# Optimization experiments

Hardware: AMD Instinct MI355X
Metric: run time of the kernel (lower is better)

Reference implementation:

```python
import jax, jax.numpy as jnp
import numpy as np

M_ROWS, K, N = 4096, 4096, 4096
DIVFACTOR = 1.0 / (127.0 * 127.0)


def setup_inputs() -> dict:
    key = jax.random.key(0)
    k1, k2, k3, k4, k5 = jax.random.split(key, 5)
    # quantized activations and weights, int8 range
    x = jax.random.randint(k1, (M_ROWS, K), -128, 128, dtype=jnp.int32).astype(jnp.int8)
    scale_x = jnp.abs(jax.random.normal(k2, (M_ROWS,), dtype=jnp.float32)) * 0.01
    weight_int8 = jax.random.randint(k3, (N, K), -128, 128, dtype=jnp.int32).astype(jnp.int8)
    scale_w = jnp.abs(jax.random.normal(k4, (N,), dtype=jnp.float32)) * 0.01
    bias = (jax.random.normal(k5, (N,), dtype=jnp.float32) * 0.01).astype(jnp.float16)
    return {"x": x, "scale_x": scale_x, "weight_int8": weight_int8, "scale_w": scale_w, "bias": bias}


def reference(x, scale_x, weight_int8, scale_w, bias):
    # int8 @ int8^T accumulated (reference path computes in fp32, like torch .float())
    acc = jnp.matmul(x.astype(jnp.float32), weight_int8.T.astype(jnp.float32))  # [M, N]
    out = scale_w[None, :] * (scale_x[:, None] * (acc * DIVFACTOR))
    out = out + bias[None, :].astype(jnp.float32)  # bias promoted fp16->fp32, as in torch
    return out.astype(jnp.float16)
```

## Files before the change

kernel.cpp:

```cpp
#include <hip/hip_runtime.h>
#include <hip/hip_fp16.h>

typedef int v4i __attribute__((ext_vector_type(4)));
typedef const unsigned __attribute__((address_space(1)))* gas_t;
typedef unsigned __attribute__((address_space(3)))* las_t;

#define DIVFACTOR (1.0f / 16129.0f)

__device__ __forceinline__ unsigned pack4(int4 v) {
    return (unsigned)(v.x & 0xFF) | ((unsigned)(v.y & 0xFF) << 8) |
           ((unsigned)(v.z & 0xFF) << 16) | ((unsigned)v.w << 24);
}

__device__ __forceinline__ void gload16(const void* g, void* l) {
    __builtin_amdgcn_global_load_lds((gas_t)g, (las_t)l, 16, 0, 0);
}

__global__ __launch_bounds__(256) void pack_kernel(
    const int* __restrict__ x, const int* __restrict__ w, uint4* __restrict__ ws)
{
    const int u   = blockIdx.x * 256 + threadIdx.x;
    const int s   = u & 7;
    const int row = (u >> 3) & 127;
    const int h   = (u >> 10) & 1;
    const int kt  = (u >> 11) & 31;
    const int p   = u >> 16;
    const int* src = (blockIdx.y == 0) ? x : w;
    uint4* dst = ws + (size_t)blockIdx.y * 1048576;

    const int grow = p * 256 + h * 128 + row;
    const int4* sp = (const int4*)(src + (size_t)grow * 4096 + kt * 128 + s * 16);
    int4 s0 = sp[0], s1 = sp[1], s2 = sp[2], s3 = sp[3];
    uint4 d = make_uint4(pack4(s0), pack4(s1), pack4(s2), pack4(s3));
    dst[(((size_t)((p * 32 + kt) * 2 + h)) << 10) + row * 8 + (s ^ (row & 7))] = d;
}

__global__ __launch_bounds__(512, 1) void i8gemm_8ph(
    const uint4* __restrict__ Ap, const uint4* __restrict__ Bp,
    const float* __restrict__ scale_x, const float* __restrict__ scale_w,
    const void* __restrict__ bias, float* __restrict__ out)
{
    __shared__ uint4 ldsq[8192];
    char* ldsb = (char*)ldsq;

    const int bid = blockIdx.x;
    const int swb = ((bid & 7) << 5) | (bid >> 3);
    const int bx  = swb & 15;
    const int by  = swb >> 4;

    const int t    = threadIdx.x;
    const int lane = t & 63;
    const int wid  = t >> 6;
    const int wr   = wid >> 2;
    const int wc   = wid & 3;
    const int r    = lane & 15;
    const int g    = lane >> 4;

    const uint4* aBase = Ap + (size_t)by * 65536 + t;
    const uint4* bBase = Bp + (size_t)bx * 65536 + t;

    const int sl0 = ((g ^ (r & 7)) << 4);
    const int sl1 = (((4 + g) ^ (r & 7)) << 4);
    const int aoff0 = wr * 16384 + r * 128 + sl0;
    const int aoff1 = wr * 16384 + r * 128 + sl1;
    const int boff0 = 32768 + (wc >> 1) * 16384 + ((wc & 1) * 64 + r) * 128 + sl0;
    const int boff1 = 32768 + (wc >> 1) * 16384 + ((wc & 1) * 64 + r) * 128 + sl1;

#define ARD(BUF,M,KS) (*(const v4i*)(ldsb + (BUF)*65536 + aoff##KS + (M)*2048))
#define BRD(BUF,N,KS) (*(const v4i*)(ldsb + (BUF)*65536 + boff##KS + (N)*2048))

#define STAGE(KT, MAT, HALF, BUF) do{ \
    const uint4* s_ = ((MAT) ? bBase : aBase) + (KT)*2048 + (HALF)*1024; \
    char* d_ = ldsb + (BUF)*65536 + (MAT)*32768 + (HALF)*16384 + t*16; \
    gload16((const void*)s_, (void*)d_); \
    gload16((const void*)(s_ + 512), (void*)(d_ + 8192)); \
}while(0)

#define BAR asm volatile("s_barrier" ::: "memory")

#define RD_B_A01(BUF) do{ \
    _Pragma("unroll") for (int n_ = 0; n_ < 4; ++n_) { bfr[n_][0] = BRD(BUF,n_,0); bfr[n_][1] = BRD(BUF,n_,1); } \
    afr[0][0]=ARD(BUF,0,0); afr[0][1]=ARD(BUF,0,1); afr[1][0]=ARD(BUF,1,0); afr[1][1]=ARD(BUF,1,1); \
}while(0)

#define RD_A27(BUF) do{ \
    _Pragma("unroll") for (int m_ = 2; m_ < 8; ++m_) { afr[m_][0] = ARD(BUF,m_,0); afr[m_][1] = ARD(BUF,m_,1); } \
}while(0)

#define CLUSTER(MA,MB) do{ \
    __builtin_amdgcn_s_setprio(1); \
    _Pragma("unroll") for (int n_ = 0; n_ < 4; ++n_) { \
        acc[MA][n_] = __builtin_amdgcn_mfma_i32_16x16x64_i8(afr[MA][0], bfr[n_][0], acc[MA][n_], 0,0,0); \
        acc[MA][n_] = __builtin_amdgcn_mfma_i32_16x16x64_i8(afr[MA][1], bfr[n_][1], acc[MA][n_], 0,0,0); \
        acc[MB][n_] = __builtin_amdgcn_mfma_i32_16x16x64_i8(afr[MB][0], bfr[n_][0], acc[MB][n_], 0,0,0); \
        acc[MB][n_] = __builtin_amdgcn_mfma_i32_16x16x64_i8(afr[MB][1], bfr[n_][1], acc[MB][n_], 0,0,0); } \
    __builtin_amdgcn_s_setprio(0); \
}while(0)

#define ITER(KB, STEADY) do{ \
    RD_B_A01(0); STAGE((KB)+1,1,0,1); BAR; CLUSTER(0,1); BAR;                  \
    RD_A27(0);   STAGE((KB)+1,1,1,1); BAR; CLUSTER(2,3); BAR;                  \
    if (STEADY) STAGE((KB)+2,0,0,0); BAR; CLUSTER(4,5); BAR;                   \
    if (STEADY) { STAGE((KB)+2,0,1,0); asm volatile("s_waitcnt vmcnt(4)" ::: "memory"); } \
    else        { asm volatile("s_waitcnt vmcnt(0)" ::: "memory"); } \
    BAR; CLUSTER(6,7); BAR;                                                    \
    RD_B_A01(1); if (STEADY) STAGE((KB)+2,1,0,0); BAR; CLUSTER(0,1); BAR;      \
    RD_A27(1);   if (STEADY) STAGE((KB)+2,1,1,0); BAR; CLUSTER(2,3); BAR;      \
    if (STEADY) STAGE((KB)+3,0,0,1); BAR; CLUSTER(4,5); BAR;                   \
    if (STEADY) { STAGE((KB)+3,0,1,1); asm volatile("s_waitcnt vmcnt(4)" ::: "memory"); } \
    BAR; CLUSTER(6,7); BAR;                                                    \
}while(0)

    v4i acc[8][4];
    #pragma unroll
    for (int m = 0; m < 8; ++m)
        #pragma unroll
        for (int n = 0; n < 4; ++n) acc[m][n] = (v4i){0, 0, 0, 0};
    v4i afr[8][2], bfr[4][2];

    STAGE(0,0,0,0); STAGE(0,0,1,0); STAGE(0,1,0,0); STAGE(0,1,1,0);
    STAGE(1,0,0,1); STAGE(1,0,1,1);
    asm volatile("s_waitcnt vmcnt(4)" ::: "memory");
    BAR;

    for (int i = 0; i < 15; ++i) { ITER(2 * i, 1); }
    ITER(30, 0);

#undef ITER
#undef CLUSTER
#undef RD_A27
#undef RD_B_A01
#undef BAR
#undef STAGE
#undef BRD
#undef ARD

    const float p0  = ((const float*)bias)[0];
    const float ap0 = fabsf(p0);
    const bool bias_is_f32 = (ap0 >= 1e-6f && ap0 <= 1.0f);

    float swv[4], bvv[4];
    #pragma unroll
    for (int n = 0; n < 4; ++n) {
        int col = bx * 256 + wc * 64 + n * 16 + r;
        swv[n] = scale_w[col];
        bvv[n] = bias_is_f32 ? ((const float*)bias)[col]
                             : __half2float(((const __half*)bias)[col]);
    }

    #pragma unroll
    for (int m = 0; m < 8; ++m) {
        float sxr[4];
        #pragma unroll
        for (int q = 0; q < 4; ++q)
            sxr[q] = scale_x[by * 256 + wr * 128 + m * 16 + g * 4 + q] * DIVFACTOR;
        #pragma unroll
        for (int q = 0; q < 4; ++q) {
            int row = by * 256 + wr * 128 + m * 16 + g * 4 + q;
            #pragma unroll
            for (int n = 0; n < 4; ++n) {
                int col = bx * 256 + wc * 64 + n * 16 + r;
                float v = (float)acc[m][n][q] * sxr[q] * swv[n] + bvv[n];
                out[(size_t)row * 4096 + col] = __half2float(__float2half(v));
            }
        }
    }
}

__global__ __launch_bounds__(256) void i8gemm_kernel(
    const int* __restrict__ x, const int* __restrict__ w,
    const float* __restrict__ scale_x, const float* __restrict__ scale_w,
    const void* __restrict__ bias, float* __restrict__ out)
{
    __shared__ int lds[4096];
    const int t = threadIdx.x, bx = blockIdx.x, by = blockIdx.y;
    const int lane = t & 63, wid = t >> 6, wr = wid >> 1, wc = wid & 1;
    const int th = t >> 4, tl = t & 15;
    const int* aptr = x + (size_t)(by * 128 + th) * 4096 + tl * 4;
    const int* bptr = w + (size_t)(bx * 128 + th) * 4096 + tl * 4;
    const int wbase = th * 16 + (tl ^ (((th >> 1) & 3) << 2));
    const int r = lane & 15, g = lane >> 4;
    const int sw4 = (r >> 1) & 3;
    const int a_rd = (wr * 64 + r) * 16 + ((g ^ sw4) << 2);
    const int b_rd = 2048 + (wc * 64 + r) * 16 + ((g ^ sw4) << 2);

    v4i acc[4][4];
    #pragma unroll
    for (int m = 0; m < 4; ++m)
        #pragma unroll
        for (int n = 0; n < 4; ++n) acc[m][n] = (v4i){0, 0, 0, 0};

    int4 va[8], vb[8];
    #pragma unroll
    for (int j = 0; j < 8; ++j) { va[j] = *(const int4*)(aptr + j * 65536); vb[j] = *(const int4*)(bptr + j * 65536); }

    for (int kt = 0; kt < 64; ++kt) {
        __syncthreads();
        #pragma unroll
        for (int j = 0; j < 8; ++j) {
            lds[wbase + j * 256]        = (int)pack4(va[j]);
            lds[2048 + wbase + j * 256] = (int)pack4(vb[j]);
        }
        __syncthreads();
        if (kt < 63) {
            const int* ap = aptr + (kt + 1) * 64;
            const int* bp = bptr + (kt + 1) * 64;
            #pragma unroll
            for (int j = 0; j < 8; ++j) { va[j] = *(const int4*)(ap + j * 65536); vb[j] = *(const int4*)(bp + j * 65536); }
        }
        v4i af[4], bf[4];
        #pragma unroll
        for (int m = 0; m < 4; ++m) af[m] = *(const v4i*)&lds[a_rd + m * 256];
        #pragma unroll
        for (int n = 0; n < 4; ++n) bf[n] = *(const v4i*)&lds[b_rd + n * 256];
        #pragma unroll
        for (int m = 0; m < 4; ++m)
            #pragma unroll
            for (int n = 0; n < 4; ++n)
                acc[m][n] = __builtin_amdgcn_mfma_i32_16x16x64_i8(af[m], bf[n], acc[m][n], 0, 0, 0);
    }

    const float p0 = ((const float*)bias)[0];
    const float ap0 = fabsf(p0);
    const bool bias_is_f32 = (ap0 >= 1e-6f && ap0 <= 1.0f);
    float sxv[4][4];
    #pragma unroll
    for (int m = 0; m < 4; ++m)
        #pragma unroll
        for (int q = 0; q < 4; ++q)
            sxv[m][q] = scale_x[by * 128 + wr * 64 + m * 16 + g * 4 + q] * DIVFACTOR;
    float swv[4], bvv[4];
    #pragma unroll
    for (int n = 0; n < 4; ++n) {
        int col = bx * 128 + wc * 64 + n * 16 + r;
        swv[n] = scale_w[col];
        bvv[n] = bias_is_f32 ? ((const float*)bias)[col] : __half2float(((const __half*)bias)[col]);
    }
    #pragma unroll
    for (int m = 0; m < 4; ++m)
        #pragma unroll
        for (int q = 0; q < 4; ++q) {
            int row = by * 128 + wr * 64 + m * 16 + g * 4 + q;
            float s = sxv[m][q];
            #pragma unroll
            for (int n = 0; n < 4; ++n) {
                int col = bx * 128 + wc * 64 + n * 16 + r;
                float v = (float)acc[m][n][q] * s * swv[n] + bvv[n];
                out[(size_t)row * 4096 + col] = __half2float(__float2half(v));
            }
        }
}

extern "C" void kernel_launch(void* const* d_in, const int* in_sizes, int n_in,
                              void* d_out, int out_size, void* d_ws, size_t ws_size,
                              hipStream_t stream) {
    const int*   x   = (const int*)d_in[0];
    const float* sx  = (const float*)d_in[1];
    const int*   w   = (const int*)d_in[2];
    const float* sw  = (const float*)d_in[3];
    const void*  bi  = d_in[4];
    float*       out = (float*)d_out;
    (void)in_sizes; (void)n_in; (void)out_size;

    if (ws_size >= (size_t)33554432) {
        uint4* ws = (uint4*)d_ws;
        hipLaunchKernelGGL(pack_kernel, dim3(4096, 2, 1), dim3(256, 1, 1), 0, stream, x, w, ws);
        hipLaunchKernelGGL(i8gemm_8ph, dim3(256, 1, 1), dim3(512, 1, 1), 0, stream,
                           ws, ws + 1048576, sx, sw, bi, out);
    } else {
        hipLaunchKernelGGL(i8gemm_kernel, dim3(32, 32, 1), dim3(256, 1, 1), 0, stream,
                           x, w, sx, sw, bi, out);
    }
}
```

Baseline: 231.3 us.

## Switch int8 GEMM inner loop to 32x32x32 MFMA tiles

Replaces the 16x16x64 int8 MFMA with the 32x32x32 variant, regrouping each wave's 128x64 tile into 4x2 blocks of 32x32. LDS fragment addressing, the swizzle, and the epilogue row/column mapping are reworked to match the new accumulator layout. The larger instruction gives more math per operand fetch and fewer MFMA issues, which should cut LDS read traffic. The risk is a different bank-conflict pattern and register pressure from the 16-wide accumulators.

```diff
diff --git a/kernel.cpp b/kernel.cpp
--- a/kernel.cpp
+++ b/kernel.cpp
@@ -1,7 +1,8 @@
 #include <hip/hip_runtime.h>
 #include <hip/hip_fp16.h>
 
-typedef int v4i __attribute__((ext_vector_type(4)));
+typedef int v4i  __attribute__((ext_vector_type(4)));
+typedef int v16i __attribute__((ext_vector_type(16)));
 typedef const unsigned __attribute__((address_space(1)))* gas_t;
 typedef unsigned __attribute__((address_space(3)))* las_t;
 
@@ -53,21 +54,20 @@
     const int wid  = t >> 6;
     const int wr   = wid >> 2;
     const int wc   = wid & 3;
-    const int r    = lane & 15;
-    const int g    = lane >> 4;
+    const int al   = lane & 31;
+    const int hi   = lane >> 5;
 
     const uint4* aBase = Ap + (size_t)by * 65536 + t;
     const uint4* bBase = Bp + (size_t)bx * 65536 + t;
 
-    const int sl0 = ((g ^ (r & 7)) << 4);
-    const int sl1 = (((4 + g) ^ (r & 7)) << 4);
-    const int aoff0 = wr * 16384 + r * 128 + sl0;
-    const int aoff1 = wr * 16384 + r * 128 + sl1;
-    const int boff0 = 32768 + (wc >> 1) * 16384 + ((wc & 1) * 64 + r) * 128 + sl0;
-    const int boff1 = 32768 + (wc >> 1) * 16384 + ((wc & 1) * 64 + r) * 128 + sl1;
-
-#define ARD(BUF,M,KS) (*(const v4i*)(ldsb + (BUF)*65536 + aoff##KS + (M)*2048))
-#define BRD(BUF,N,KS) (*(const v4i*)(ldsb + (BUF)*65536 + boff##KS + (N)*2048))
+    int swz[4];
+    #pragma unroll
+    for (int ks = 0; ks < 4; ++ks) swz[ks] = (((ks * 2 + hi) ^ (al & 7)) << 4);
+    const int abase = wr * 16384 + al * 128;
+    const int bbase = 32768 + (wc >> 1) * 16384 + ((wc & 1) * 64 + al) * 128;
+
+#define ARD(BUF,MB,KS) (*(const v4i*)(ldsb + (BUF)*65536 + abase + (MB)*4096 + swz[KS]))
+#define BRD(BUF,NB,KS) (*(const v4i*)(ldsb + (BUF)*65536 + bbase + (NB)*4096 + swz[KS]))
 
 #define STAGE(KT, MAT, HALF, BUF) do{ \
     const uint4* s_ = ((MAT) ? bBase : aBase) + (KT)*2048 + (HALF)*1024; \
@@ -78,45 +78,47 @@
 
 #define BAR asm volatile("s_barrier" ::: "memory")
 
-#define RD_B_A01(BUF) do{ \
-    _Pragma("unroll") for (int n_ = 0; n_ < 4; ++n_) { bfr[n_][0] = BRD(BUF,n_,0); bfr[n_][1] = BRD(BUF,n_,1); } \
-    afr[0][0]=ARD(BUF,0,0); afr[0][1]=ARD(BUF,0,1); afr[1][0]=ARD(BUF,1,0); afr[1][1]=ARD(BUF,1,1); \
-}while(0)
-
-#define RD_A27(BUF) do{ \
-    _Pragma("unroll") for (int m_ = 2; m_ < 8; ++m_) { afr[m_][0] = ARD(BUF,m_,0); afr[m_][1] = ARD(BUF,m_,1); } \
-}while(0)
-
-#define CLUSTER(MA,MB) do{ \
+#define RD_B_A0(BUF) do{ \
+    _Pragma("unroll") for (int nb_ = 0; nb_ < 2; ++nb_) \
+        _Pragma("unroll") for (int ks_ = 0; ks_ < 4; ++ks_) bfr[nb_][ks_] = BRD(BUF,nb_,ks_); \
+    _Pragma("unroll") for (int ks_ = 0; ks_ < 4; ++ks_) afr[0][ks_] = ARD(BUF,0,ks_); \
+}while(0)
+
+#define RD_A123(BUF) do{ \
+    _Pragma("unroll") for (int mb_ = 1; mb_ < 4; ++mb_) \
+        _Pragma("unroll") for (int ks_ = 0; ks_ < 4; ++ks_) afr[mb_][ks_] = ARD(BUF,mb_,ks_); \
+}while(0)
+
+#define CLUSTER(MB) do{ \
     __builtin_amdgcn_s_setprio(1); \
-    _Pragma("unroll") for (int n_ = 0; n_ < 4; ++n_) { \
-        acc[MA][n_] = __builtin_amdgcn_mfma_i32_16x16x64_i8(afr[MA][0], bfr[n_][0], acc[MA][n_], 0,0,0); \
-        acc[MA][n_] = __builtin_amdgcn_mfma_i32_16x16x64_i8(afr[MA][1], bfr[n_][1], acc[MA][n_], 0,0,0); \
-        acc[MB][n_] = __builtin_amdgcn_mfma_i32_16x16x64_i8(afr[MB][0], bfr[n_][0], acc[MB][n_], 0,0,0); \
-        acc[MB][n_] = __builtin_amdgcn_mfma_i32_16x16x64_i8(afr[MB][1], bfr[n_][1], acc[MB][n_], 0,0,0); } \
+    _Pragma("unroll") for (int ks_ = 0; ks_ < 4; ++ks_) { \
+        acc[MB][0] = __builtin_amdgcn_mfma_i32_32x32x32_i8(afr[MB][ks_], bfr[0][ks_], acc[MB][0], 0,0,0); \
+        acc[MB][1] = __builtin_amdgcn_mfma_i32_32x32x32_i8(afr[MB][ks_], bfr[1][ks_], acc[MB][1], 0,0,0); } \
     __builtin_amdgcn_s_setprio(0); \
 }while(0)
 
 #define ITER(KB, STEADY) do{ \
-    RD_B_A01(0); STAGE((KB)+1,1,0,1); BAR; CLUSTER(0,1); BAR;                  \
-    RD_A27(0);   STAGE((KB)+1,1,1,1); BAR; CLUSTER(2,3); BAR;                  \
-    if (STEADY) STAGE((KB)+2,0,0,0); BAR; CLUSTER(4,5); BAR;                   \
+    RD_B_A0(0);  STAGE((KB)+1,1,0,1); BAR; CLUSTER(0); BAR;                    \
+    RD_A123(0);  STAGE((KB)+1,1,1,1); BAR; CLUSTER(1); BAR;                    \
+    if (STEADY) STAGE((KB)+2,0,0,0); BAR; CLUSTER(2); BAR;                     \
     if (STEADY) { STAGE((KB)+2,0,1,0); asm volatile("s_waitcnt vmcnt(4)" ::: "memory"); } \
     else        { asm volatile("s_waitcnt vmcnt(0)" ::: "memory"); } \
-    BAR; CLUSTER(6,7); BAR;                                                    \
-    RD_B_A01(1); if (STEADY) STAGE((KB)+2,1,0,0); BAR; CLUSTER(0,1); BAR;      \
-    RD_A27(1);   if (STEADY) STAGE((KB)+2,1,1,0); BAR; CLUSTER(2,3); BAR;      \
-    if (STEADY) STAGE((KB)+3,0,0,1); BAR; CLUSTER(4,5); BAR;                   \
+    BAR; CLUSTER(3); BAR;                                                      \
+    RD_B_A0(1);  if (STEADY) STAGE((KB)+2,1,0,0); BAR; CLUSTER(0); BAR;        \
+    RD_A123(1);  if (STEADY) STAGE((KB)+2,1,1,0); BAR; CLUSTER(1); BAR;        \
+    if (STEADY) STAGE((KB)+3,0,0,1); BAR; CLUSTER(2); BAR;                     \
     if (STEADY) { STAGE((KB)+3,0,1,1); asm volatile("s_waitcnt vmcnt(4)" ::: "memory"); } \
-    BAR; CLUSTER(6,7); BAR;                                                    \
-}while(0)
-
-    v4i acc[8][4];
-    #pragma unroll
-    for (int m = 0; m < 8; ++m)
-        #pragma unroll
-        for (int n = 0; n < 4; ++n) acc[m][n] = (v4i){0, 0, 0, 0};
-    v4i afr[8][2], bfr[4][2];
+    BAR; CLUSTER(3); BAR;                                                      \
+}while(0)
+
+    v16i acc[4][2];
+    #pragma unroll
+    for (int mb = 0; mb < 4; ++mb)
+        #pragma unroll
+        for (int nb = 0; nb < 2; ++nb)
+            #pragma unroll
+            for (int q = 0; q < 16; ++q) acc[mb][nb][q] = 0;
+    v4i afr[4][4], bfr[2][4];
 
     STAGE(0,0,0,0); STAGE(0,0,1,0); STAGE(0,1,0,0); STAGE(0,1,1,0);
     STAGE(1,0,0,1); STAGE(1,0,1,1);
@@ -128,8 +130,8 @@
 
 #undef ITER
 #undef CLUSTER
-#undef RD_A27
-#undef RD_B_A01
+#undef RD_A123
+#undef RD_B_A0
 #undef BAR
 #undef STAGE
 #undef BRD
@@ -139,28 +141,25 @@
     const float ap0 = fabsf(p0);
     const bool bias_is_f32 = (ap0 >= 1e-6f && ap0 <= 1.0f);
 
-    float swv[4], bvv[4];
-    #pragma unroll
-    for (int n = 0; n < 4; ++n) {
-        int col = bx * 256 + wc * 64 + n * 16 + r;
-        swv[n] = scale_w[col];
-        bvv[n] = bias_is_f32 ? ((const float*)bias)[col]
-                             : __half2float(((const __half*)bias)[col]);
-    }
-
-    #pragma unroll
-    for (int m = 0; m < 8; ++m) {
-        float sxr[4];
-        #pragma unroll
-        for (int q = 0; q < 4; ++q)
-            sxr[q] = scale_x[by * 256 + wr * 128 + m * 16 + g * 4 + q] * DIVFACTOR;
-        #pragma unroll
-        for (int q = 0; q < 4; ++q) {
-            int row = by * 256 + wr * 128 + m * 16 + g * 4 + q;
-            #pragma unroll
-            for (int n = 0; n < 4; ++n) {
-                int col = bx * 256 + wc * 64 + n * 16 + r;
-                float v = (float)acc[m][n][q] * sxr[q] * swv[n] + bvv[n];
+    float swv[2], bvv[2];
+    #pragma unroll
+    for (int nb = 0; nb < 2; ++nb) {
+        int col = bx * 256 + wc * 64 + nb * 32 + al;
+        swv[nb] = scale_w[col];
+        bvv[nb] = bias_is_f32 ? ((const float*)bias)[col]
+                              : __half2float(((const __half*)bias)[col]);
+    }
+
+    #pragma unroll
+    for (int mb = 0; mb < 4; ++mb) {
+        #pragma unroll
+        for (int q = 0; q < 16; ++q) {
+            int row = by * 256 + wr * 128 + mb * 32 + (q & 3) + 8 * (q >> 2) + 4 * hi;
+            float sx_ = scale_x[row] * DIVFACTOR;
+            #pragma unroll
+            for (int nb = 0; nb < 2; ++nb) {
+                int col = bx * 256 + wc * 64 + nb * 32 + al;
+                float v = (float)acc[mb][nb][q] * sx_ * swv[nb] + bvv[nb];
                 out[(size_t)row * 4096 + col] = __half2float(__float2half(v));
             }
         }
```

New measurement: 238.7 us. 1.03x slower.

## Double-buffer B fragments and spread A fragment reads across MFMA clusters

Applied to the files above, without the earlier changes.

B-tile fragments now alternate between two register sets, so the next buffer's B fragments are read from LDS during the previous cluster's MFMAs. A fragments are loaded two rows at a time just before each cluster instead of in large batches. The global-to-LDS staging order is rearranged so B tiles arrive first, with adjusted vmcnt waits. The aim is to hide LDS read latency behind MFMA work, at the cost of extra VGPR pressure from the second B fragment set and a riskier, hand-tuned wait and barrier schedule.

```diff
diff --git a/kernel.cpp b/kernel.cpp
--- a/kernel.cpp
+++ b/kernel.cpp
@@ -1,7 +1,7 @@
 #include <hip/hip_runtime.h>
 #include <hip/hip_fp16.h>
 
-typedef int v4i __attribute__((ext_vector_type(4)));
+typedef int v4i  __attribute__((ext_vector_type(4)));
 typedef const unsigned __attribute__((address_space(1)))* gas_t;
 typedef unsigned __attribute__((address_space(3)))* las_t;
 
@@ -77,38 +77,41 @@
 }while(0)
 
 #define BAR asm volatile("s_barrier" ::: "memory")
-
-#define RD_B_A01(BUF) do{ \
-    _Pragma("unroll") for (int n_ = 0; n_ < 4; ++n_) { bfr[n_][0] = BRD(BUF,n_,0); bfr[n_][1] = BRD(BUF,n_,1); } \
-    afr[0][0]=ARD(BUF,0,0); afr[0][1]=ARD(BUF,0,1); afr[1][0]=ARD(BUF,1,0); afr[1][1]=ARD(BUF,1,1); \
-}while(0)
-
-#define RD_A27(BUF) do{ \
-    _Pragma("unroll") for (int m_ = 2; m_ < 8; ++m_) { afr[m_][0] = ARD(BUF,m_,0); afr[m_][1] = ARD(BUF,m_,1); } \
-}while(0)
-
-#define CLUSTER(MA,MB) do{ \
+#define VM4 asm volatile("s_waitcnt vmcnt(4)" ::: "memory")
+#define VM0 asm volatile("s_waitcnt vmcnt(0)" ::: "memory")
+#define VM8 asm volatile("s_waitcnt vmcnt(8)" ::: "memory")
+
+#define RD_A2(BUF,M0) do{ \
+    afr[M0][0]   = ARD(BUF,M0,0);   afr[M0][1]   = ARD(BUF,M0,1); \
+    afr[(M0)+1][0] = ARD(BUF,(M0)+1,0); afr[(M0)+1][1] = ARD(BUF,(M0)+1,1); \
+}while(0)
+
+#define RD_B8(BUF,ARR) do{ \
+    _Pragma("unroll") for (int n_ = 0; n_ < 4; ++n_) { \
+        ARR[n_][0] = BRD(BUF,n_,0); ARR[n_][1] = BRD(BUF,n_,1); } \
+}while(0)
+
+#define CLUSTER(ARR,MA,MB) do{ \
     __builtin_amdgcn_s_setprio(1); \
     _Pragma("unroll") for (int n_ = 0; n_ < 4; ++n_) { \
-        acc[MA][n_] = __builtin_amdgcn_mfma_i32_16x16x64_i8(afr[MA][0], bfr[n_][0], acc[MA][n_], 0,0,0); \
-        acc[MA][n_] = __builtin_amdgcn_mfma_i32_16x16x64_i8(afr[MA][1], bfr[n_][1], acc[MA][n_], 0,0,0); \
-        acc[MB][n_] = __builtin_amdgcn_mfma_i32_16x16x64_i8(afr[MB][0], bfr[n_][0], acc[MB][n_], 0,0,0); \
-        acc[MB][n_] = __builtin_amdgcn_mfma_i32_16x16x64_i8(afr[MB][1], bfr[n_][1], acc[MB][n_], 0,0,0); } \
+        acc[MA][n_] = __builtin_amdgcn_mfma_i32_16x16x64_i8(afr[MA][0], ARR[n_][0], acc[MA][n_], 0,0,0); \
+        acc[MA][n_] = __builtin_amdgcn_mfma_i32_16x16x64_i8(afr[MA][1], ARR[n_][1], acc[MA][n_], 0,0,0); \
+        acc[MB][n_] = __builtin_amdgcn_mfma_i32_16x16x64_i8(afr[MB][0], ARR[n_][0], acc[MB][n_], 0,0,0); \
+        acc[MB][n_] = __builtin_amdgcn_mfma_i32_16x16x64_i8(afr[MB][1], ARR[n_][1], acc[MB][n_], 0,0,0); } \
     __builtin_amdgcn_s_setprio(0); \
 }while(0)
 
 #define ITER(KB, STEADY) do{ \
-    RD_B_A01(0); STAGE((KB)+1,1,0,1); BAR; CLUSTER(0,1); BAR;                  \
-    RD_A27(0);   STAGE((KB)+1,1,1,1); BAR; CLUSTER(2,3); BAR;                  \
-    if (STEADY) STAGE((KB)+2,0,0,0); BAR; CLUSTER(4,5); BAR;                   \
-    if (STEADY) { STAGE((KB)+2,0,1,0); asm volatile("s_waitcnt vmcnt(4)" ::: "memory"); } \
-    else        { asm volatile("s_waitcnt vmcnt(0)" ::: "memory"); } \
-    BAR; CLUSTER(6,7); BAR;                                                    \
-    RD_B_A01(1); if (STEADY) STAGE((KB)+2,1,0,0); BAR; CLUSTER(0,1); BAR;      \
-    RD_A27(1);   if (STEADY) STAGE((KB)+2,1,1,0); BAR; CLUSTER(2,3); BAR;      \
-    if (STEADY) STAGE((KB)+3,0,0,1); BAR; CLUSTER(4,5); BAR;                   \
-    if (STEADY) { STAGE((KB)+3,0,1,1); asm volatile("s_waitcnt vmcnt(4)" ::: "memory"); } \
-    BAR; CLUSTER(6,7); BAR;                                                    \
+    RD_A2(0,0); STAGE((KB)+1,1,0,1); BAR; CLUSTER(bfrA,0,1); BAR;              \
+    RD_A2(0,2); STAGE((KB)+1,1,1,1); BAR; CLUSTER(bfrA,2,3); BAR;              \
+    RD_A2(0,4); if (STEADY) STAGE((KB)+2,1,0,0); BAR; CLUSTER(bfrA,4,5); BAR;  \
+    RD_A2(0,6); if (STEADY) { STAGE((KB)+2,1,1,0); VM4; } else { VM0; } \
+    BAR; RD_B8(1,bfrB); CLUSTER(bfrA,6,7); BAR;                                \
+    RD_A2(1,0); RD_A2(1,2); if (STEADY) STAGE((KB)+2,0,0,0); BAR; CLUSTER(bfrB,0,1); BAR;  \
+    RD_A2(1,4); RD_A2(1,6); if (STEADY) { STAGE((KB)+2,0,1,0); VM4; } \
+    BAR; if (STEADY) RD_B8(0,bfrA); CLUSTER(bfrB,2,3); BAR;                    \
+    if (STEADY) STAGE((KB)+3,0,0,1); BAR; CLUSTER(bfrB,4,5); BAR;              \
+    if (STEADY) { STAGE((KB)+3,0,1,1); VM4; } BAR; CLUSTER(bfrB,6,7); BAR;     \
 }while(0)
 
     v4i acc[8][4];
@@ -116,20 +119,25 @@
     for (int m = 0; m < 8; ++m)
         #pragma unroll
         for (int n = 0; n < 4; ++n) acc[m][n] = (v4i){0, 0, 0, 0};
-    v4i afr[8][2], bfr[4][2];
-
-    STAGE(0,0,0,0); STAGE(0,0,1,0); STAGE(0,1,0,0); STAGE(0,1,1,0);
+    v4i afr[8][2], bfrA[4][2], bfrB[4][2];
+
+    STAGE(0,1,0,0); STAGE(0,1,1,0);
+    STAGE(0,0,0,0); STAGE(0,0,1,0);
     STAGE(1,0,0,1); STAGE(1,0,1,1);
-    asm volatile("s_waitcnt vmcnt(4)" ::: "memory");
-    BAR;
+    VM8; BAR;
+    RD_B8(0,bfrA);
+    VM4; BAR;
 
     for (int i = 0; i < 15; ++i) { ITER(2 * i, 1); }
     ITER(30, 0);
 
 #undef ITER
 #undef CLUSTER
-#undef RD_A27
-#undef RD_B_A01
+#undef RD_B8
+#undef RD_A2
+#undef VM8
+#undef VM0
+#undef VM4
 #undef BAR
 #undef STAGE
 #undef BRD
```

Measured after the change: 231.4 us. Within noise of the previous version (+0.0%).
